# Kernel tuning notes

Hardware: AMD Instinct MI355X
Metric: run time of the kernel (lower is better)

Reference implementation:

```python
import jax, jax.numpy as jnp
import numpy as np

TOP_K = 50
TEMPERATURE = 1.0
RENORMALIZE = True


def setup_inputs() -> dict:
    key = jax.random.key(0)
    k1, k2 = jax.random.split(key)
    B, T, V, D = 4, 128, 128000, 2048
    logits = jax.random.normal(k1, (B, T, V), dtype=jnp.float32)
    emb_weight = jax.random.normal(k2, (V, D), dtype=jnp.float32)
    return {"logits": logits, "emb_weight": emb_weight}


def reference(logits, emb_weight):
    # probs = softmax(logits / temperature) over vocab
    probs = jax.nn.softmax(logits / TEMPERATURE, axis=-1)          # [B,T,V]
    topk_w, topk_idx = jax.lax.top_k(probs, TOP_K)                 # [B,T,k]
    if RENORMALIZE:
        topk_w = topk_w / jnp.sum(topk_w, axis=-1, keepdims=True)
    emb = emb_weight[topk_idx]                                     # [B,T,k,D]
    soft_emb = jnp.einsum('btk,btkd->btd', topk_w, emb)            # [B,T,D]
    return soft_emb
```

## Files before the change

### kernel.cpp

```cpp
#include <hip/hip_runtime.h>
#include <math.h>

#define VOCAB  128000
#define DIM    2048
#define TOPK   50
#define NTHR   512
#define CAP    512
#define NBINS  4096
#define THRESH 3.0f

typedef float f4 __attribute__((ext_vector_type(4)));

__global__ __launch_bounds__(NTHR, 4) void softmix_kernel(
    const float* __restrict__ logits,
    const float* __restrict__ emb,
    float* __restrict__ out)
{
    __shared__ float cand_v[CAP];
    __shared__ int   cand_i[CAP];
    __shared__ unsigned int cand_cnt;
    __shared__ float sel_v[TOPK];
    __shared__ int   sel_i[TOPK];
    __shared__ float sel_w[TOPK];
    __shared__ float wsum;
    __shared__ unsigned int hist[NBINS];
    __shared__ unsigned int seg[NTHR];
    __shared__ unsigned int binStar;

    const int row = blockIdx.x;
    const int t   = threadIdx.x;
    const f4* lrow = (const f4*)(logits + (size_t)row * VOCAB);
    const int n4 = VOCAB / 4;

    if (t == 0) cand_cnt = 0u;
    __syncthreads();

    #pragma unroll 1
    for (int it = 0; it < 15; ++it) {
        const int p0 = t + it * (4 * NTHR);
        f4 v0 = __builtin_nontemporal_load(lrow + p0);
        f4 v1 = __builtin_nontemporal_load(lrow + p0 + NTHR);
        f4 v2 = __builtin_nontemporal_load(lrow + p0 + 2 * NTHR);
        f4 v3 = __builtin_nontemporal_load(lrow + p0 + 3 * NTHR);
        #pragma unroll
        for (int j = 0; j < 4; ++j) {
            float f = v0[j];
            if (f >= THRESH) {
                unsigned pos = atomicAdd(&cand_cnt, 1u);
                if (pos < CAP) { cand_v[pos] = f; cand_i[pos] = 4 * p0 + j; }
            }
        }
        #pragma unroll
        for (int j = 0; j < 4; ++j) {
            float f = v1[j];
            if (f >= THRESH) {
                unsigned pos = atomicAdd(&cand_cnt, 1u);
                if (pos < CAP) { cand_v[pos] = f; cand_i[pos] = 4 * (p0 + NTHR) + j; }
            }
        }
        #pragma unroll
        for (int j = 0; j < 4; ++j) {
            float f = v2[j];
            if (f >= THRESH) {
                unsigned pos = atomicAdd(&cand_cnt, 1u);
                if (pos < CAP) { cand_v[pos] = f; cand_i[pos] = 4 * (p0 + 2 * NTHR) + j; }
            }
        }
        #pragma unroll
        for (int j = 0; j < 4; ++j) {
            float f = v3[j];
            if (f >= THRESH) {
                unsigned pos = atomicAdd(&cand_cnt, 1u);
                if (pos < CAP) { cand_v[pos] = f; cand_i[pos] = 4 * (p0 + 3 * NTHR) + j; }
            }
        }
    }
    #pragma unroll 1
    for (int p = 15 * (4 * NTHR) + t; p < n4; p += NTHR) {
        f4 v = __builtin_nontemporal_load(lrow + p);
        #pragma unroll
        for (int j = 0; j < 4; ++j) {
            float f = v[j];
            if (f >= THRESH) {
                unsigned pos = atomicAdd(&cand_cnt, 1u);
                if (pos < CAP) { cand_v[pos] = f; cand_i[pos] = 4 * p + j; }
            }
        }
    }
    __syncthreads();

    int C = (int)cand_cnt;

    if (C < TOPK || C > CAP) {
        for (int i = t; i < NBINS; i += NTHR) hist[i] = 0u;
        if (t == 0) cand_cnt = 0u;
        __syncthreads();
        for (int p = t; p < n4; p += NTHR) {
            f4 v = lrow[p];
            #pragma unroll
            for (int j = 0; j < 4; ++j) {
                unsigned u = __float_as_uint(v[j]);
                unsigned key = (u & 0x80000000u) ? ~u : (u | 0x80000000u);
                atomicAdd(&hist[key >> 20], 1u);
            }
        }
        __syncthreads();
        {
            const int per = NBINS / NTHR;
            const int base = t * per;
            unsigned s = 0;
            for (int i = 0; i < per; ++i) s += hist[base + i];
            seg[t] = s;
            __syncthreads();
            unsigned suff = 0;
            for (int j = NTHR - 1; j > t; --j) suff += seg[j];
            if (suff < TOPK && suff + seg[t] >= TOPK) {
                unsigned running = suff;
                for (int b = per - 1; b >= 0; --b) {
                    unsigned c = hist[base + b];
                    if (running + c >= TOPK) { binStar = (unsigned)(base + b); break; }
                    running += c;
                }
            }
        }
        __syncthreads();
        const unsigned bstar = binStar;
        for (int p = t; p < n4; p += NTHR) {
            f4 v = lrow[p];
            #pragma unroll
            for (int j = 0; j < 4; ++j) {
                float f = v[j];
                unsigned u = __float_as_uint(f);
                unsigned key = (u & 0x80000000u) ? ~u : (u | 0x80000000u);
                if ((key >> 20) >= bstar) {
                    unsigned pos = atomicAdd(&cand_cnt, 1u);
                    if (pos < CAP) { cand_v[pos] = f; cand_i[pos] = 4 * p + j; }
                }
            }
        }
        __syncthreads();
        C = (cand_cnt < (unsigned)CAP) ? (int)cand_cnt : CAP;
    }

    for (int i = t; i < C; i += NTHR) {
        float vi = cand_v[i]; int ii = cand_i[i];
        int rank = 0;
        for (int j = 0; j < C; ++j) {
            float vj = cand_v[j]; int ij = cand_i[j];
            rank += (int)((vj > vi) || (vj == vi && ij < ii));
        }
        if (rank < TOPK) { sel_v[rank] = vi; sel_i[rank] = ii; }
    }
    __syncthreads();

    if (t < 64) {
        float p = 0.f;
        if (t < TOPK) { p = expf(sel_v[t] - sel_v[0]); sel_w[t] = p; }
        for (int off = 32; off; off >>= 1) p += __shfl_down(p, off);
        if (t == 0) wsum = p;
    }
    __syncthreads();
    const float inv = 1.0f / wsum;

    float4 accA = {0.f, 0.f, 0.f, 0.f};
    float4 accB = {0.f, 0.f, 0.f, 0.f};
    #pragma unroll 1
    for (int k = 0; k < TOPK; k += 2) {
        const float wA = sel_w[k];
        const float wB = sel_w[k + 1];
        const float4* erA = (const float4*)(emb + (size_t)sel_i[k] * DIM);
        const float4* erB = (const float4*)(emb + (size_t)sel_i[k + 1] * DIM);
        float4 eA = erA[t];
        float4 eB = erB[t];
        accA.x += wA * eA.x; accA.y += wA * eA.y; accA.z += wA * eA.z; accA.w += wA * eA.w;
        accB.x += wB * eB.x; accB.y += wB * eB.y; accB.z += wB * eB.z; accB.w += wB * eB.w;
    }
    float4 acc;
    acc.x = (accA.x + accB.x) * inv;
    acc.y = (accA.y + accB.y) * inv;
    acc.z = (accA.z + accB.z) * inv;
    acc.w = (accA.w + accB.w) * inv;

    f4 accv = { acc.x, acc.y, acc.z, acc.w };
    f4* orow = (f4*)(out + (size_t)row * DIM);
    __builtin_nontemporal_store(accv, orow + t);
}

extern "C" void kernel_launch(void* const* d_in, const int* in_sizes, int n_in,
                              void* d_out, int out_size, void* d_ws, size_t ws_size,
                              hipStream_t stream) {
    const float* logits = (const float*)d_in[0];
    const float* emb    = (const float*)d_in[1];
    float* out = (float*)d_out;
    const int rows = in_sizes[0] / VOCAB;
    softmix_kernel<<<rows, NTHR, 0, stream>>>(logits, emb, out);
}
```

Measured before the change: 87.34 us.

## Use 1024-thread blocks and split embedding gather across two halves

Doubles the block size to 1024 threads and retunes the unrolled scan loop so each thread covers fewer logits per row. The weighted embedding gather is split so the two 512-thread halves handle alternating pairs of top-k rows, and the partial sums are combined through shared memory by reusing the histogram buffer. The aim is more parallelism per row for the memory-bound scan and the gather, since there are only 512 blocks. In exchange it adds an extra barrier and shared-memory reduction, and the larger block may limit occupancy.

```diff
diff --git a/kernel.cpp b/kernel.cpp
--- a/kernel.cpp
+++ b/kernel.cpp
@@ -4,14 +4,14 @@
 #define VOCAB  128000
 #define DIM    2048
 #define TOPK   50
-#define NTHR   512
+#define NTHR   1024
 #define CAP    512
 #define NBINS  4096
 #define THRESH 3.0f
 
 typedef float f4 __attribute__((ext_vector_type(4)));
 
-__global__ __launch_bounds__(NTHR, 4) void softmix_kernel(
+__global__ __launch_bounds__(NTHR, 8) void softmix_kernel(
     const float* __restrict__ logits,
     const float* __restrict__ emb,
     float* __restrict__ out)
@@ -36,7 +36,7 @@
     __syncthreads();
 
     #pragma unroll 1
-    for (int it = 0; it < 15; ++it) {
+    for (int it = 0; it < 7; ++it) {
         const int p0 = t + it * (4 * NTHR);
         f4 v0 = __builtin_nontemporal_load(lrow + p0);
         f4 v1 = __builtin_nontemporal_load(lrow + p0 + NTHR);
@@ -76,7 +76,7 @@
         }
     }
     #pragma unroll 1
-    for (int p = 15 * (4 * NTHR) + t; p < n4; p += NTHR) {
+    for (int p = 7 * (4 * NTHR) + t; p < n4; p += NTHR) {
         f4 v = __builtin_nontemporal_load(lrow + p);
         #pragma unroll
         for (int j = 0; j < 4; ++j) {
@@ -162,28 +162,40 @@
     __syncthreads();
     const float inv = 1.0f / wsum;
 
+    const int tt   = t & 511;
+    const int half = t >> 9;
     float4 accA = {0.f, 0.f, 0.f, 0.f};
     float4 accB = {0.f, 0.f, 0.f, 0.f};
     #pragma unroll 1
-    for (int k = 0; k < TOPK; k += 2) {
-        const float wA = sel_w[k];
-        const float wB = sel_w[k + 1];
-        const float4* erA = (const float4*)(emb + (size_t)sel_i[k] * DIM);
-        const float4* erB = (const float4*)(emb + (size_t)sel_i[k + 1] * DIM);
-        float4 eA = erA[t];
-        float4 eB = erB[t];
+    for (int pp = half; pp < TOPK / 2; pp += 2) {
+        const int kA = 2 * pp, kB = 2 * pp + 1;
+        const float wA = sel_w[kA];
+        const float wB = sel_w[kB];
+        const float4* erA = (const float4*)(emb + (size_t)sel_i[kA] * DIM);
+        const float4* erB = (const float4*)(emb + (size_t)sel_i[kB] * DIM);
+        float4 eA = erA[tt];
+        float4 eB = erB[tt];
         accA.x += wA * eA.x; accA.y += wA * eA.y; accA.z += wA * eA.z; accA.w += wA * eA.w;
         accB.x += wB * eB.x; accB.y += wB * eB.y; accB.z += wB * eB.z; accB.w += wB * eB.w;
     }
-    float4 acc;
-    acc.x = (accA.x + accB.x) * inv;
-    acc.y = (accA.y + accB.y) * inv;
-    acc.z = (accA.z + accB.z) * inv;
-    acc.w = (accA.w + accB.w) * inv;
-
-    f4 accv = { acc.x, acc.y, acc.z, acc.w };
-    f4* orow = (f4*)(out + (size_t)row * DIM);
-    __builtin_nontemporal_store(accv, orow + t);
+    float4* red = (float4*)hist;
+    if (half == 1) {
+        float4 s;
+        s.x = accA.x + accB.x; s.y = accA.y + accB.y;
+        s.z = accA.z + accB.z; s.w = accA.w + accB.w;
+        red[tt] = s;
+    }
+    __syncthreads();
+    if (half == 0) {
+        float4 r = red[tt];
+        f4 accv;
+        accv[0] = (accA.x + accB.x + r.x) * inv;
+        accv[1] = (accA.y + accB.y + r.y) * inv;
+        accv[2] = (accA.z + accB.z + r.z) * inv;
+        accv[3] = (accA.w + accB.w + r.w) * inv;
+        f4* orow = (f4*)(out + (size_t)row * DIM);
+        __builtin_nontemporal_store(accv, orow + tt);
+    }
 }
 
 extern "C" void kernel_launch(void* const* d_in, const int* in_sizes, int n_in,
```

New measurement: 79.86 us. -8.6%, faster.
